# Performance work log

Measured on AMD Instinct MI355X. Metric: run time of the kernel, lower is better.

The kernel has to match this reference:

```python
import jax, jax.numpy as jnp
import numpy as np

B, D, H, O, E, K = 8192, 1024, 4096, 1024, 8, 2

def setup_inputs() -> dict:
    key = jax.random.key(0)
    ks = jax.random.split(key, 8)
    x = jax.random.normal(ks[0], (B, D), dtype=jnp.float32)
    topk_idx = jax.random.randint(ks[1], (B, K), 0, E, dtype=jnp.int32)
    weights = jax.random.uniform(ks[2], (B, K), dtype=jnp.float32)
    s1 = 1.0 / np.sqrt(D)
    s2 = 1.0 / np.sqrt(H)
    W1 = jax.random.uniform(ks[3], (E, D, H), minval=-s1, maxval=s1, dtype=jnp.float32)
    b1 = jax.random.uniform(ks[4], (E, H), minval=-s1, maxval=s1, dtype=jnp.float32)
    W2 = jax.random.uniform(ks[5], (E, H, O), minval=-s2, maxval=s2, dtype=jnp.float32)
    b2 = jax.random.uniform(ks[6], (E, O), minval=-s2, maxval=s2, dtype=jnp.float32)
    return {"x": x, "topk_idx": topk_idx, "weights": weights,
            "W1": W1, "b1": b1, "W2": W2, "b2": b2}

def reference(x, topk_idx, weights, W1, b1, W2, b2):
    # Per-token gate mass for each expert: gate[b,e] = sum_i weights[b,i]*[topk_idx[b,i]==e]
    # Equivalent to the original masked gather/scatter combine (duplicates in topk_idx sum).
    out = jnp.zeros((x.shape[0], W2.shape[-1]), dtype=x.dtype)
    for e in range(W1.shape[0]):  # small fixed loop over experts
        gate_e = jnp.sum(weights * (topk_idx == e), axis=1)  # [B]
        h = jax.nn.relu(x @ W1[e] + b1[e])                   # [B,H]
        out_e = h @ W2[e] + b2[e]                            # [B,O]
        out = out + gate_e[:, None] * out_e
    return out
```

## Files before the change

### kernel.cpp

```cpp
#include <hip/hip_runtime.h>
#include <stdint.h>

#define B_TOK 8192
#define D_DIM 1024
#define H_DIM 4096
#define O_DIM 1024
#define E_NUM 8
#define K_TOP 2
#define NPAIR (B_TOK * K_TOP)

typedef short bf16x8 __attribute__((ext_vector_type(8)));
typedef float f32x4 __attribute__((ext_vector_type(4)));

struct Hdr {
    int counts[8];
    int offsets[9];
    int cursor[8];
    int total1, total2;
    int base1[9];
    int base2[9];
};

__device__ __forceinline__ unsigned short f2bf(float f) {
    union { float f; unsigned int u; } v; v.f = f;
    unsigned int u = v.u;
    unsigned int r = (u + 0x7fffu + ((u >> 16) & 1u)) >> 16;
    return (unsigned short)r;
}

__device__ __forceinline__ float bf2f(unsigned short s) {
    union { unsigned int u; float f; } v;
    v.u = ((unsigned int)s) << 16;
    return v.f;
}

__device__ __forceinline__ void async16(const void* g, const void* l) {
    __builtin_amdgcn_global_load_lds(
        (__attribute__((address_space(1))) void*)(uintptr_t)g,
        (__attribute__((address_space(3))) void*)(uint32_t)(uintptr_t)l,
        16, 0, 0);
}


__global__ void cvt_x_kernel(const float* __restrict__ x, unsigned short* __restrict__ xb) {
    int i = (blockIdx.x * 256 + threadIdx.x) * 4;
    float4 v = *(const float4*)(x + i);
    ushort4 o;
    o.x = f2bf(v.x); o.y = f2bf(v.y); o.z = f2bf(v.z); o.w = f2bf(v.w);
    *(ushort4*)(xb + i) = o;
}

__global__ __launch_bounds__(256) void tconv_kernel(const float* __restrict__ in,
                                                    unsigned short* __restrict__ out,
                                                    int R, int C) {
    __shared__ float t[64 * 69];
    int e = blockIdx.z;
    const float* ip = in + (size_t)e * R * C;
    unsigned short* op = out + (size_t)e * R * C;
    int c0 = blockIdx.x * 64, r0 = blockIdx.y * 64;
    int tid = threadIdx.x;
    int lr = tid >> 4;
    int lc = (tid & 15) * 4;
#pragma unroll
    for (int i = 0; i < 4; i++) {
        int row = lr + i * 16;
        float4 v = *(const float4*)&ip[(size_t)(r0 + row) * C + c0 + lc];
        t[row * 69 + lc + 0] = v.x;
        t[row * 69 + lc + 1] = v.y;
        t[row * 69 + lc + 2] = v.z;
        t[row * 69 + lc + 3] = v.w;
    }
    __syncthreads();
#pragma unroll
    for (int i = 0; i < 4; i++) {
        int c = lr + i * 16;
        ushort4 o;
        o.x = f2bf(t[(lc + 0) * 69 + c]);
        o.y = f2bf(t[(lc + 1) * 69 + c]);
        o.z = f2bf(t[(lc + 2) * 69 + c]);
        o.w = f2bf(t[(lc + 3) * 69 + c]);
        *(ushort4*)&op[(size_t)(c0 + c) * R + r0 + lc] = o;
    }
}


__global__ void route_count_kernel(const int* __restrict__ topk, Hdr* hdr) {
    __shared__ int cnt[8];
    int tid = threadIdx.x;
    if (tid < 8) cnt[tid] = 0;
    __syncthreads();
    for (int i = tid; i < NPAIR; i += 1024) atomicAdd(&cnt[topk[i]], 1);
    __syncthreads();
    if (tid == 0) {
        int off = 0, t1 = 0, t2 = 0;
        for (int e = 0; e < 8; e++) {
            int c = cnt[e];
            hdr->counts[e] = c;
            hdr->offsets[e] = off;
            hdr->cursor[e] = off;
            hdr->base1[e] = t1;
            hdr->base2[e] = t2;
            int mt = (c + 127) >> 7;
            t1 += mt * (H_DIM / 128);
            t2 += mt * (O_DIM / 128);
            off += c;
        }
        hdr->offsets[8] = off;
        hdr->base1[8] = t1;
        hdr->base2[8] = t2;
        hdr->total1 = t1;
        hdr->total2 = t2;
    }
}

__global__ void route_fill_kernel(const int* __restrict__ topk, const float* __restrict__ wts,
                                  Hdr* hdr, int* __restrict__ ptok, float* __restrict__ pgate,
                                  int* __restrict__ pslot) {
    int i = blockIdx.x * 256 + threadIdx.x;
    int e = topk[i];
    int pos = atomicAdd(&hdr->cursor[e], 1);
    ptok[pos] = i >> 1;
    pgate[pos] = wts[i];
    pslot[i] = pos;
}

__global__ void ws_fail_kernel(float* out) { out[0] = 1.0e9f; }

template <int K, int N, bool GATHER>
__global__ __launch_bounds__(256, 4) void moe_gemm_kernel(
    const unsigned short* __restrict__ A,
    const unsigned short* __restrict__ Bt,
    const float* __restrict__ bias,
    const Hdr* __restrict__ hdr,
    const int* __restrict__ ptok,
    unsigned short* __restrict__ outp) {

    __shared__ __align__(16) unsigned short smem[128 * 132];
    unsigned short* As = smem;
    unsigned short* Bs = smem + 128 * 64;

    const int tid = threadIdx.x;
    const int lane = tid & 63;
    const int wv = tid >> 6;
    const int wu = __builtin_amdgcn_readfirstlane(wv);
    const int wm = (wv & 1) * 64;
    const int wn = (wv >> 1) * 64;
    const int lr = lane & 15;
    const int lkg = lane >> 4;

    const int total = GATHER ? hdr->total1 : hdr->total2;
    const int* tb = GATHER ? hdr->base1 : hdr->base2;
    constexpr int NT = N / 128;

    int chunk = (total + 7) >> 3;
    int seq = (blockIdx.x & 7) * chunk + (blockIdx.x >> 3);
    if (seq >= total) return;

    int e = 0;
#pragma unroll
    for (int j = 1; j < 8; j++)
        if (seq >= tb[j]) e = j;
    e = __builtin_amdgcn_readfirstlane(e);
    int lt = seq - tb[e];
    int cnt = hdr->counts[e], off = hdr->offsets[e];
    int MT = (cnt + 127) >> 7;

    int band = lt / (NT * 8);
    int r = lt - band * (NT * 8);
    int mrem = MT - band * 8;
    mrem = mrem > 8 ? 8 : mrem;
    int gsz = mrem * 8;
    int g = r / gsz;
    int rg = r - g * gsz;
    int gm = rg % mrem;
    int gn = rg / mrem;
    int mtile = band * 8 + gm;
    int ntile = g * 8 + gn;
    int m0 = mtile * 128, n0 = ntile * 128;

    const char* Ab = (const char*)A;
    const char* Bb = (const char*)(Bt + (size_t)e * ((size_t)N * K));
    uint32_t offA[4], offB[4];
#pragma unroll
    for (int i = 0; i < 4; i++) {
        int s = i * 256 + tid;
        int rr = s >> 3;
        int cl = (s & 7) ^ (rr & 7);
        int p = off + m0 + rr;
        p = p > NPAIR - 1 ? NPAIR - 1 : p;
        uint32_t row = GATHER ? (uint32_t)ptok[p] : (uint32_t)p;
        offA[i] = (row * (uint32_t)K + (uint32_t)cl * 8u) * 2u;
        offB[i] = (((uint32_t)(n0 + rr)) * (uint32_t)K + (uint32_t)cl * 8u) * 2u;
    }

    f32x4 zero = {0.f, 0.f, 0.f, 0.f};
    f32x4 acc[4][4];
#pragma unroll
    for (int mt = 0; mt < 4; mt++)
#pragma unroll
        for (int nt = 0; nt < 4; nt++) acc[mt][nt] = zero;

    for (int k0 = 0; k0 < K; k0 += 64) {
#pragma unroll
        for (int i = 0; i < 4; i++) {
            async16(Ab + offA[i], &As[(i * 256 + wu * 64) * 8]);
            async16(Bb + offB[i], &Bs[(i * 256 + wu * 64) * 8]);
            offA[i] += 128;
            offB[i] += 128;
        }
        __syncthreads();
#pragma unroll
        for (int ks = 0; ks < 2; ks++) {
            bf16x8 af[4];
#pragma unroll
            for (int q = 0; q < 4; q++) {
                int ra = wm + q * 16 + lr;
                int ca = (ks * 4 + lkg) ^ (ra & 7);
                af[q] = *(const bf16x8*)&As[ra * 64 + ca * 8];
            }
#pragma unroll
            for (int nt = 0; nt < 4; nt++) {
                int rb = wn + nt * 16 + lr;
                int cb = (ks * 4 + lkg) ^ (rb & 7);
                bf16x8 bfr = *(const bf16x8*)&Bs[rb * 64 + cb * 8];
#pragma unroll
                for (int mt = 0; mt < 4; mt++)
                    acc[mt][nt] = __builtin_amdgcn_mfma_f32_16x16x32_bf16(
                        af[mt], bfr, acc[mt][nt], 0, 0, 0);
            }
        }
        __syncthreads();
    }

#pragma unroll
    for (int nt = 0; nt < 4; nt++) {
        int n = wn + nt * 16 + lr;
        float bv = bias[(size_t)e * N + n0 + n];
#pragma unroll
        for (int mt = 0; mt < 4; mt++) {
#pragma unroll
            for (int r2 = 0; r2 < 4; r2++) {
                int m = wm + mt * 16 + lkg * 4 + r2;
                float v = acc[mt][nt][r2] + bv;
                if (GATHER) v = v > 0.f ? v : 0.f;
                smem[m * 132 + n] = f2bf(v);
            }
        }
    }
    __syncthreads();
    int rows_valid = cnt - m0;
    if (rows_valid > 128) rows_valid = 128;
#pragma unroll
    for (int j = 0; j < 16; j++) {
        int idx = j * 256 + tid;
        int row = idx >> 5;
        int lc8 = idx & 31;
        if (row < rows_valid) {
            uint2 v = *(const uint2*)&smem[row * 132 + lc8 * 4];
            *(uint2*)&outp[(size_t)(off + m0 + row) * N + n0 + lc8 * 4] = v;
        }
    }
}

__global__ void combine_kernel(const unsigned short* __restrict__ oslot,
                               const int* __restrict__ pslot,
                               const float* __restrict__ wts,
                               float* __restrict__ out) {
    int tok = blockIdx.x;
    int s0 = pslot[tok * 2], s1 = pslot[tok * 2 + 1];
    float g0 = wts[tok * 2], g1 = wts[tok * 2 + 1];
    int n = threadIdx.x * 4;
    ushort4 a = *(const ushort4*)&oslot[(size_t)s0 * O_DIM + n];
    ushort4 b = *(const ushort4*)&oslot[(size_t)s1 * O_DIM + n];
    float4 o;
    o.x = g0 * bf2f(a.x) + g1 * bf2f(b.x);
    o.y = g0 * bf2f(a.y) + g1 * bf2f(b.y);
    o.z = g0 * bf2f(a.z) + g1 * bf2f(b.z);
    o.w = g0 * bf2f(a.w) + g1 * bf2f(b.w);
    *(float4*)&out[(size_t)tok * O_DIM + n] = o;
}


extern "C" void kernel_launch(void* const* d_in, const int* in_sizes, int n_in,
                              void* d_out, int out_size, void* d_ws, size_t ws_size,
                              hipStream_t stream) {
    const float* x   = (const float*)d_in[0];
    const int* topk  = (const int*)d_in[1];
    const float* wts = (const float*)d_in[2];
    const float* W1  = (const float*)d_in[3];
    const float* b1  = (const float*)d_in[4];
    const float* W2  = (const float*)d_in[5];
    const float* b2  = (const float*)d_in[6];
    float* out = (float*)d_out;

    char* ws = (char*)d_ws;
    size_t off = 0;
    auto alloc = [&](size_t bytes) -> void* {
        void* p = ws + off;
        off += (bytes + 255) & ~(size_t)255;
        return p;
    };
    Hdr* hdr = (Hdr*)alloc(sizeof(Hdr));
    int* ptok = (int*)alloc((size_t)NPAIR * 4);
    float* pgate = (float*)alloc((size_t)NPAIR * 4);
    int* pslot = (int*)alloc((size_t)NPAIR * 4);
    unsigned short* xb   = (unsigned short*)alloc((size_t)B_TOK * D_DIM * 2);
    unsigned short* W1bt = (unsigned short*)alloc((size_t)E_NUM * D_DIM * H_DIM * 2);
    unsigned short* W2bt = (unsigned short*)alloc((size_t)E_NUM * H_DIM * O_DIM * 2);
    unsigned short* hbuf = (unsigned short*)alloc((size_t)NPAIR * H_DIM * 2);
    unsigned short* oslot = W1bt;

    if (off > ws_size) {
        hipMemsetAsync(d_out, 0, (size_t)out_size * sizeof(float), stream);
        ws_fail_kernel<<<1, 1, 0, stream>>>(out);
        return;
    }

    cvt_x_kernel<<<(B_TOK * D_DIM) / 1024, 256, 0, stream>>>(x, xb);
    tconv_kernel<<<dim3(H_DIM / 64, D_DIM / 64, E_NUM), dim3(256), 0, stream>>>(W1, W1bt, D_DIM, H_DIM);
    tconv_kernel<<<dim3(O_DIM / 64, H_DIM / 64, E_NUM), dim3(256), 0, stream>>>(W2, W2bt, H_DIM, O_DIM);
    route_count_kernel<<<1, 1024, 0, stream>>>(topk, hdr);
    route_fill_kernel<<<NPAIR / 256, 256, 0, stream>>>(topk, wts, hdr, ptok, pgate, pslot);

    moe_gemm_kernel<D_DIM, H_DIM, true><<<4608, 256, 0, stream>>>(
        xb, W1bt, b1, hdr, ptok, hbuf);
    moe_gemm_kernel<H_DIM, O_DIM, false><<<1152, 256, 0, stream>>>(
        hbuf, W2bt, b2, hdr, ptok, oslot);
    combine_kernel<<<B_TOK, 256, 0, stream>>>(oslot, pslot, wts, out);
}
```

Measured before the change: 753.3 us.

## Rewrite MoE grouped GEMM with 256x256 tiles and double-buffered async pipeline

The grouped GEMM now uses 256x256 output tiles with 512 threads (8 waves) and 128KB of dynamic shared memory. K-slices are split into halves and double-buffered, so global-to-LDS async loads run ahead of the MFMA phases, with explicit vmcnt waits, barriers and setprio. The aim is more data reuse per tile and hiding load latency behind matrix math. In exchange occupancy drops to about one block per CU, the grid is much smaller, and the simpler tile ordering loses the grouped L2 swizzle.

```diff
diff --git a/kernel.cpp b/kernel.cpp
--- a/kernel.cpp
+++ b/kernel.cpp
@@ -100,9 +100,9 @@
             hdr->cursor[e] = off;
             hdr->base1[e] = t1;
             hdr->base2[e] = t2;
-            int mt = (c + 127) >> 7;
-            t1 += mt * (H_DIM / 128);
-            t2 += mt * (O_DIM / 128);
+            int mt = (c + 255) >> 8;
+            t1 += mt * (H_DIM / 256);
+            t2 += mt * (O_DIM / 256);
             off += c;
         }
         hdr->offsets[8] = off;
@@ -126,8 +126,67 @@
 
 __global__ void ws_fail_kernel(float* out) { out[0] = 1.0e9f; }
 
-template <int K, int N, bool GATHER>
-__global__ __launch_bounds__(256, 4) void moe_gemm_kernel(
+
+#define ASL(BUF, KH) ((BUF) * 32768 + (KH) * 16384)
+
+#define STG_A(BUF, KH, KOFF) do { \
+    async16(Ab + srcA[0] + (KOFF), smem + ASL(BUF, KH) + wu * 2048); \
+    async16(Ab + srcA[1] + (KOFF), smem + ASL(BUF, KH) + wu * 2048 + 1024); } while (0)
+
+#define STG_B(BUF, KH, KOFF) do { \
+    async16(Bb + srcB[0] + (KOFF), smem + 65536 + ASL(BUF, KH) + wu * 2048); \
+    async16(Bb + srcB[1] + (KOFF), smem + 65536 + ASL(BUF, KH) + wu * 2048 + 1024); } while (0)
+
+#define VM6 asm volatile("s_waitcnt vmcnt(6)" ::: "memory")
+#define VM0 asm volatile("s_waitcnt vmcnt(0)" ::: "memory")
+#define NOPX ((void)0)
+
+#define PHASE0(BUF, KH, STAGE, CKPT) do { \
+    STAGE; \
+    bq[0] = *(const bf16x8*)&smem[pBo[0] + ASL(BUF, KH)]; \
+    bq[1] = *(const bf16x8*)&smem[pBo[1] + ASL(BUF, KH)]; \
+    bq[2] = *(const bf16x8*)&smem[pBo[2] + ASL(BUF, KH)]; \
+    bq[3] = *(const bf16x8*)&smem[pBo[3] + ASL(BUF, KH)]; \
+    aq[0] = *(const bf16x8*)&smem[pAo[0] + ASL(BUF, KH)]; \
+    aq[1] = *(const bf16x8*)&smem[pAo[1] + ASL(BUF, KH)]; \
+    aq[2] = *(const bf16x8*)&smem[pAo[2] + ASL(BUF, KH)]; \
+    aq[3] = *(const bf16x8*)&smem[pAo[3] + ASL(BUF, KH)]; \
+    __builtin_amdgcn_s_barrier(); \
+    asm volatile("s_waitcnt lgkmcnt(0)" ::: "memory"); \
+    __builtin_amdgcn_s_setprio(1); \
+    _Pragma("unroll") \
+    for (int q_ = 0; q_ < 4; ++q_) { \
+        _Pragma("unroll") \
+        for (int n_ = 0; n_ < 4; ++n_) \
+            acc[q_][n_] = __builtin_amdgcn_mfma_f32_16x16x32_bf16(aq[q_], bq[n_], acc[q_][n_], 0, 0, 0); \
+    } \
+    __builtin_amdgcn_s_setprio(0); \
+    CKPT; \
+    __builtin_amdgcn_s_barrier(); \
+} while (0)
+
+#define PHASE1(BUF, KH, STAGE, CKPT) do { \
+    STAGE; \
+    aq[0] = *(const bf16x8*)&smem[pAo[4] + ASL(BUF, KH)]; \
+    aq[1] = *(const bf16x8*)&smem[pAo[5] + ASL(BUF, KH)]; \
+    aq[2] = *(const bf16x8*)&smem[pAo[6] + ASL(BUF, KH)]; \
+    aq[3] = *(const bf16x8*)&smem[pAo[7] + ASL(BUF, KH)]; \
+    __builtin_amdgcn_s_barrier(); \
+    asm volatile("s_waitcnt lgkmcnt(0)" ::: "memory"); \
+    __builtin_amdgcn_s_setprio(1); \
+    _Pragma("unroll") \
+    for (int q_ = 0; q_ < 4; ++q_) { \
+        _Pragma("unroll") \
+        for (int n_ = 0; n_ < 4; ++n_) \
+            acc[4 + q_][n_] = __builtin_amdgcn_mfma_f32_16x16x32_bf16(aq[q_], bq[n_], acc[4 + q_][n_], 0, 0, 0); \
+    } \
+    __builtin_amdgcn_s_setprio(0); \
+    CKPT; \
+    __builtin_amdgcn_s_barrier(); \
+} while (0)
+
+template <int KD, int N, bool GATHER>
+__global__ __launch_bounds__(512, 2) void moe_gemm_kernel(
     const unsigned short* __restrict__ A,
     const unsigned short* __restrict__ Bt,
     const float* __restrict__ bias,
@@ -135,22 +194,22 @@
     const int* __restrict__ ptok,
     unsigned short* __restrict__ outp) {
 
-    __shared__ __align__(16) unsigned short smem[128 * 132];
-    unsigned short* As = smem;
-    unsigned short* Bs = smem + 128 * 64;
+    extern __shared__ __align__(16) char smem[];
+    constexpr int NT = KD / 64;
+    constexpr int NI = NT / 2;
+    static_assert(NT >= 4 && (NT % 2) == 0, "K-tile count");
 
     const int tid = threadIdx.x;
     const int lane = tid & 63;
     const int wv = tid >> 6;
     const int wu = __builtin_amdgcn_readfirstlane(wv);
-    const int wm = (wv & 1) * 64;
-    const int wn = (wv >> 1) * 64;
     const int lr = lane & 15;
     const int lkg = lane >> 4;
+    const int wr = wv >> 2;
+    const int wc = wv & 3;
 
     const int total = GATHER ? hdr->total1 : hdr->total2;
     const int* tb = GATHER ? hdr->base1 : hdr->base2;
-    constexpr int NT = N / 128;
 
     int chunk = (total + 7) >> 3;
     int seq = (blockIdx.x & 7) * chunk + (blockIdx.x >> 3);
@@ -163,101 +222,103 @@
     e = __builtin_amdgcn_readfirstlane(e);
     int lt = seq - tb[e];
     int cnt = hdr->counts[e], off = hdr->offsets[e];
-    int MT = (cnt + 127) >> 7;
-
-    int band = lt / (NT * 8);
-    int r = lt - band * (NT * 8);
-    int mrem = MT - band * 8;
-    mrem = mrem > 8 ? 8 : mrem;
-    int gsz = mrem * 8;
-    int g = r / gsz;
-    int rg = r - g * gsz;
-    int gm = rg % mrem;
-    int gn = rg / mrem;
-    int mtile = band * 8 + gm;
-    int ntile = g * 8 + gn;
-    int m0 = mtile * 128, n0 = ntile * 128;
+    int MT = (cnt + 255) >> 8;
+    int mtile = lt % MT, ntile = lt / MT;
+    int m0 = mtile * 256, n0 = ntile * 256;
 
     const char* Ab = (const char*)A;
-    const char* Bb = (const char*)(Bt + (size_t)e * ((size_t)N * K));
-    uint32_t offA[4], offB[4];
-#pragma unroll
-    for (int i = 0; i < 4; i++) {
-        int s = i * 256 + tid;
-        int rr = s >> 3;
-        int cl = (s & 7) ^ (rr & 7);
-        int p = off + m0 + rr;
-        p = p > NPAIR - 1 ? NPAIR - 1 : p;
-        uint32_t row = GATHER ? (uint32_t)ptok[p] : (uint32_t)p;
-        offA[i] = (row * (uint32_t)K + (uint32_t)cl * 8u) * 2u;
-        offB[i] = (((uint32_t)(n0 + rr)) * (uint32_t)K + (uint32_t)cl * 8u) * 2u;
-    }
-
-    f32x4 zero = {0.f, 0.f, 0.f, 0.f};
-    f32x4 acc[4][4];
-#pragma unroll
-    for (int mt = 0; mt < 4; mt++)
-#pragma unroll
-        for (int nt = 0; nt < 4; nt++) acc[mt][nt] = zero;
-
-    for (int k0 = 0; k0 < K; k0 += 64) {
-#pragma unroll
-        for (int i = 0; i < 4; i++) {
-            async16(Ab + offA[i], &As[(i * 256 + wu * 64) * 8]);
-            async16(Bb + offB[i], &Bs[(i * 256 + wu * 64) * 8]);
-            offA[i] += 128;
-            offB[i] += 128;
-        }
-        __syncthreads();
-#pragma unroll
-        for (int ks = 0; ks < 2; ks++) {
-            bf16x8 af[4];
-#pragma unroll
-            for (int q = 0; q < 4; q++) {
-                int ra = wm + q * 16 + lr;
-                int ca = (ks * 4 + lkg) ^ (ra & 7);
-                af[q] = *(const bf16x8*)&As[ra * 64 + ca * 8];
-            }
-#pragma unroll
-            for (int nt = 0; nt < 4; nt++) {
-                int rb = wn + nt * 16 + lr;
-                int cb = (ks * 4 + lkg) ^ (rb & 7);
-                bf16x8 bfr = *(const bf16x8*)&Bs[rb * 64 + cb * 8];
-#pragma unroll
-                for (int mt = 0; mt < 4; mt++)
-                    acc[mt][nt] = __builtin_amdgcn_mfma_f32_16x16x32_bf16(
-                        af[mt], bfr, acc[mt][nt], 0, 0, 0);
+    const char* Bb = (const char*)(Bt + (size_t)e * ((size_t)N * KD));
+
+    uint32_t srcA[2], srcB[2];
+#pragma unroll
+    for (int l = 0; l < 2; ++l) {
+        int p = wv * 128 + l * 64 + lane;
+        int rp = p >> 2, cp = p & 3;
+        int r = rp ^ ((rp >> 2) & 1);
+        int c = cp ^ (r & 3);
+        int q = off + m0 + r;
+        q = q > NPAIR - 1 ? NPAIR - 1 : q;
+        uint32_t rowA = GATHER ? (uint32_t)ptok[q] : (uint32_t)q;
+        srcA[l] = rowA * (uint32_t)(KD * 2) + (uint32_t)(c * 16);
+        srcB[l] = (uint32_t)(n0 + r) * (uint32_t)(KD * 2) + (uint32_t)(c * 16);
+    }
+
+    uint32_t pAo[8], pBo[4];
+#pragma unroll
+    for (int mr = 0; mr < 8; ++mr) {
+        int r = wr * 128 + mr * 16 + lr;
+        pAo[mr] = (uint32_t)((r ^ ((r >> 2) & 1)) * 64 + (lkg ^ (r & 3)) * 16);
+    }
+#pragma unroll
+    for (int nr = 0; nr < 4; ++nr) {
+        int r = wc * 64 + nr * 16 + lr;
+        pBo[nr] = (uint32_t)(65536 + (r ^ ((r >> 2) & 1)) * 64 + (lkg ^ (r & 3)) * 16);
+    }
+
+    f32x4 acc[8][4];
+#pragma unroll
+    for (int i = 0; i < 8; ++i)
+#pragma unroll
+        for (int j = 0; j < 4; ++j)
+            acc[i][j] = (f32x4){0.f, 0.f, 0.f, 0.f};
+    bf16x8 aq[4], bq[4];
+
+    STG_A(0, 0, 0u);   STG_B(0, 0, 0u);
+    STG_A(0, 1, 64u);  STG_B(0, 1, 64u);
+    STG_A(1, 0, 128u); STG_B(1, 0, 128u);
+    STG_B(1, 1, 192u);
+    VM0;
+    __builtin_amdgcn_s_barrier();
+
+    for (int it = 0; it < NI - 1; ++it) {
+        const uint32_t kb = (uint32_t)it * 256u;
+        PHASE0(0, 0, STG_A(1, 1, kb + 192u), NOPX);
+        PHASE1(0, 0, STG_B(0, 0, kb + 256u), NOPX);
+        PHASE0(0, 1, STG_A(0, 0, kb + 256u), NOPX);
+        PHASE1(0, 1, STG_B(0, 1, kb + 320u), VM6);
+        PHASE0(1, 0, STG_A(0, 1, kb + 320u), NOPX);
+        PHASE1(1, 0, STG_B(1, 0, kb + 384u), NOPX);
+        PHASE0(1, 1, STG_A(1, 0, kb + 384u), NOPX);
+        PHASE1(1, 1, STG_B(1, 1, kb + 448u), VM6);
+    }
+    {
+        const uint32_t kb = (uint32_t)(NI - 1) * 256u;
+        PHASE0(0, 0, STG_A(1, 1, kb + 192u), NOPX);
+        PHASE1(0, 0, NOPX, NOPX);
+        PHASE0(0, 1, NOPX, NOPX);
+        PHASE1(0, 1, NOPX, VM0);
+        PHASE0(1, 0, NOPX, NOPX);
+        PHASE1(1, 0, NOPX, NOPX);
+        PHASE0(1, 1, NOPX, NOPX);
+        PHASE1(1, 1, NOPX, NOPX);
+    }
+
+    int rows_valid = cnt - m0;
+    if (rows_valid > 256) rows_valid = 256;
+#pragma unroll
+    for (int nr = 0; nr < 4; ++nr) {
+        int n = wc * 64 + nr * 16 + lr;
+        float bv = bias[(size_t)e * N + n0 + n];
+#pragma unroll
+        for (int mr = 0; mr < 8; ++mr) {
+#pragma unroll
+            for (int r2 = 0; r2 < 4; ++r2) {
+                int m = wr * 128 + mr * 16 + lkg * 4 + r2;
+                float v = acc[mr][nr][r2] + bv;
+                if (GATHER) v = v > 0.f ? v : 0.f;
+                *(unsigned short*)&smem[(m * 256 + n) * 2] = f2bf(v);
             }
         }
-        __syncthreads();
-    }
-
-#pragma unroll
-    for (int nt = 0; nt < 4; nt++) {
-        int n = wn + nt * 16 + lr;
-        float bv = bias[(size_t)e * N + n0 + n];
-#pragma unroll
-        for (int mt = 0; mt < 4; mt++) {
-#pragma unroll
-            for (int r2 = 0; r2 < 4; r2++) {
-                int m = wm + mt * 16 + lkg * 4 + r2;
-                float v = acc[mt][nt][r2] + bv;
-                if (GATHER) v = v > 0.f ? v : 0.f;
-                smem[m * 132 + n] = f2bf(v);
-            }
-        }
     }
     __syncthreads();
-    int rows_valid = cnt - m0;
-    if (rows_valid > 128) rows_valid = 128;
-#pragma unroll
-    for (int j = 0; j < 16; j++) {
-        int idx = j * 256 + tid;
+#pragma unroll
+    for (int j = 0; j < 16; ++j) {
+        int idx = j * 512 + tid;
         int row = idx >> 5;
-        int lc8 = idx & 31;
+        int c16 = idx & 31;
         if (row < rows_valid) {
-            uint2 v = *(const uint2*)&smem[row * 132 + lc8 * 4];
-            *(uint2*)&outp[(size_t)(off + m0 + row) * N + n0 + lc8 * 4] = v;
+            uint4 v = *(const uint4*)&smem[row * 512 + c16 * 16];
+            *(uint4*)&outp[(size_t)(off + m0 + row) * N + n0 + c16 * 8] = v;
         }
     }
 }
@@ -316,15 +377,26 @@
         return;
     }
 
+    static int attr_done = 0;
+    if (!attr_done) {
+        (void)hipFuncSetAttribute(
+            reinterpret_cast<const void*>(&moe_gemm_kernel<D_DIM, H_DIM, true>),
+            hipFuncAttributeMaxDynamicSharedMemorySize, 131072);
+        (void)hipFuncSetAttribute(
+            reinterpret_cast<const void*>(&moe_gemm_kernel<H_DIM, O_DIM, false>),
+            hipFuncAttributeMaxDynamicSharedMemorySize, 131072);
+        attr_done = 1;
+    }
+
     cvt_x_kernel<<<(B_TOK * D_DIM) / 1024, 256, 0, stream>>>(x, xb);
     tconv_kernel<<<dim3(H_DIM / 64, D_DIM / 64, E_NUM), dim3(256), 0, stream>>>(W1, W1bt, D_DIM, H_DIM);
     tconv_kernel<<<dim3(O_DIM / 64, H_DIM / 64, E_NUM), dim3(256), 0, stream>>>(W2, W2bt, H_DIM, O_DIM);
     route_count_kernel<<<1, 1024, 0, stream>>>(topk, hdr);
     route_fill_kernel<<<NPAIR / 256, 256, 0, stream>>>(topk, wts, hdr, ptok, pgate, pslot);
 
-    moe_gemm_kernel<D_DIM, H_DIM, true><<<4608, 256, 0, stream>>>(
+    moe_gemm_kernel<D_DIM, H_DIM, true><<<1152, 512, 131072, stream>>>(
         xb, W1bt, b1, hdr, ptok, hbuf);
-    moe_gemm_kernel<H_DIM, O_DIM, false><<<1152, 256, 0, stream>>>(
+    moe_gemm_kernel<H_DIM, O_DIM, false><<<288, 512, 131072, stream>>>(
         hbuf, W2bt, b2, hdr, ptok, oslot);
     combine_kernel<<<B_TOK, 256, 0, stream>>>(oslot, pslot, wts, out);
 }
```

Measured after the change: 802.8 us. 6.6% more time.
